# Kernel optimization log

Measured on AMD Instinct MI355X. Metric: run time of the kernel, lower is better.

## Reference

```python
import jax, jax.numpy as jnp
import numpy as np

N = 32768
DEG = 9        # 8 neighbors + self-loop
B = 8
K = 3          # Chebyshev degree
IN_CH = 8
OUT_CH = 2
HID = 64


def setup_inputs() -> dict:
    key = jax.random.key(0)
    ks = jax.random.split(key, 14)
    # structured 9-neighbor stencil (CSR-like sorted rows), honoring graph sparsity
    offs = np.arange(-4, 5)
    rows_np = np.repeat(np.arange(N), DEG).astype(np.int32)
    cols_np = ((rows_np.reshape(N, DEG) + offs[None, :]) % N).reshape(-1).astype(np.int32)
    vals = jax.random.normal(ks[0], (N * DEG,), jnp.float32) * 0.1
    x = jax.random.normal(ks[1], (B, N, IN_CH), jnp.float32)

    def w(k, fin, fout):
        return jax.random.normal(k, (K * fin, fout), jnp.float32) * 0.05

    def b(k, fout):
        return jax.random.normal(k, (fout,), jnp.float32) * 0.01

    return dict(
        x=x, rows=jnp.asarray(rows_np), cols=jnp.asarray(cols_np), vals=vals,
        W1=w(ks[2], IN_CH, HID), b1=b(ks[3], HID),
        W2=w(ks[4], HID, HID), b2=b(ks[5], HID),
        W3=w(ks[6], HID, HID), b3=b(ks[7], HID),
        W4=w(ks[8], HID, HID), b4=b(ks[9], HID),
        W5=w(ks[10], HID, OUT_CH), b5=b(ks[11], OUT_CH),
    )


def _spmm(rows, cols, vals, x):
    # sparse Laplacian @ x ; x: [B, N, C] -> [B, N, C]
    g = x[:, cols, :] * vals[None, :, None]          # [B, nnz, C]
    g = jnp.swapaxes(g, 0, 1)                        # [nnz, B, C]
    y = jax.ops.segment_sum(g, rows, num_segments=N) # [N, B, C]
    return jnp.swapaxes(y, 0, 1)


def _cheb_conv(rows, cols, vals, x, W, b):
    # Chebyshev recursion: T0 = x, T1 = L x, Tk = 2 L T_{k-1} - T_{k-2}
    x0 = x
    xs = [x0]
    if K > 1:
        x1 = _spmm(rows, cols, vals, x0)
        xs.append(x1)
        for _ in range(K - 2):
            x2 = 2.0 * _spmm(rows, cols, vals, x1) - x0
            xs.append(x2)
            x0, x1 = x1, x2
    xk = jnp.concatenate(xs, axis=-1)                # [B, N, K*Fin]
    return jnp.einsum('bnf,fo->bno', xk, W) + b


def reference(x, rows, cols, vals, W1, b1, W2, b2, W3, b3, W4, b4, W5, b5):
    h = jax.nn.elu(_cheb_conv(rows, cols, vals, x, W1, b1))
    h = jax.nn.elu(_cheb_conv(rows, cols, vals, h, W2, b2))
    h = jax.nn.elu(_cheb_conv(rows, cols, vals, h, W3, b3))
    h = jax.nn.elu(_cheb_conv(rows, cols, vals, h, W4, b4))
    out = _cheb_conv(rows, cols, vals, h, W5, b5)    # no ELU on last layer
    return out
```

## Files before the change

### kernel.cpp

```cpp
#include <hip/hip_runtime.h>
#include <math.h>

#define N_PIX 32768
#define DEG 9
#define BATCH 8
#define TILE 64

typedef unsigned short u16;
typedef __attribute__((ext_vector_type(8))) short bf16x8;
typedef __attribute__((ext_vector_type(16))) float f32x16;

__device__ __forceinline__ u16 bf16_rn(float x) {
    unsigned int u = __builtin_bit_cast(unsigned int, x);
    u += 0x7fffu + ((u >> 16) & 1u);
    return (u16)(u >> 16);
}
__device__ __forceinline__ float bf16_to_f(u16 u) {
    unsigned int v = ((unsigned int)u) << 16;
    return __builtin_bit_cast(float, v);
}


__global__ void prep_wt(const float* __restrict__ W2, const float* __restrict__ W3,
                        const float* __restrict__ W4, u16* __restrict__ out) {
    const float* W = (blockIdx.x == 0) ? W2 : (blockIdx.x == 1) ? W3 : W4;
    u16* o = out + (size_t)blockIdx.x * 24576;
    const int base = blockIdx.y * 768;
    for (int idx = base + threadIdx.x; idx < base + 768; idx += 256) {
        int j = idx & 7;
        int lane = (idx >> 3) & 63;
        int rest = idx >> 9;
        int s = rest & 3, tt = rest >> 2;
        int mt = tt & 1, mat = tt >> 1;
        int k = s * 16 + (lane >> 5) * 8 + j;
        int m = mt * 32 + (lane & 31);
        float x = (mat == 0) ? W[k * 64 + m] - W[(128 + k) * 64 + m]
                : (mat == 1) ? W[(64 + k) * 64 + m]
                             : W[(128 + k) * 64 + m];
        u16 hi = bf16_rn(x);
        o[idx] = hi;
        o[12288 + idx] = bf16_rn(x - bf16_to_f(hi));
    }
}

__global__ void prep_w1(const float* __restrict__ W1, u16* __restrict__ out) {
    u16* o = out + 73728;
    const int base = blockIdx.x * 1536;
    for (int e = base + threadIdx.x; e < base + 1536 && e < 24576; e += 256) {
        int j = e & 7;
        int lane = (e >> 3) & 63;
        int tt = e >> 12;
        int mt = tt & 1, mat = tt >> 1;
        int m = mt * 32 + (lane & 31);
        float x = 0.f;
        if ((lane >> 5) == 0) {
            x = (mat == 0) ? W1[j * 64 + m] - W1[(16 + j) * 64 + m]
              : (mat == 1) ? W1[(8 + j) * 64 + m]
                           : W1[(16 + j) * 64 + m];
        }
        u16 hi = bf16_rn(x);
        o[e] = hi;
        o[24576 + e] = bf16_rn(x - bf16_to_f(hi));
    }
}

template<bool FIRST>
__global__ __launch_bounds__(512, 6)
void cheb_conv(const float* __restrict__ Xf, const u16* __restrict__ Xh,
               const u16* __restrict__ Xl, const float* __restrict__ vals,
               const u16* __restrict__ wt, int wbase, const float* __restrict__ bias,
               u16* __restrict__ Yh, u16* __restrict__ Yl) {
    constexpr int LD = 68;
    __shared__ alignas(16) float P2s[80 * LD];
    __shared__ alignas(16) float P1s[72 * LD];
    __shared__ alignas(16) float Vs[72 * 12];

    const int tid = threadIdx.x;
    const int bx = ((blockIdx.x & 7) << 6) | (blockIdx.x >> 3);
    const int n0 = bx * TILE;
    const int b  = blockIdx.y;
    const size_t bplane = (size_t)b * ((size_t)N_PIX * 64);

    for (int i = tid; i < 648; i += 512) {
        int sr = i / 9, j = i - sr * 9;
        int g = (n0 - 4 + sr) & (N_PIX - 1);
        Vs[sr * 12 + j] = vals[(size_t)g * DEG + j];
    }

    const int w = tid >> 6, lane = tid & 63;
    const int half = lane >> 5, m31 = lane & 31;

    auto gemm_accs = [&](int mat, int rowoff, int rl, f32x16& acc0, f32x16& acc1) {
        const int g = (n0 + rowoff + rl) & (N_PIX - 1);
        constexpr int SC   = FIRST ? 1 : 4;
        constexpr int LOFF = FIRST ? 24576 : 12288;
        const u16* a0p = wt + wbase + lane * 8 + (FIRST ? (mat * 2) * 4096 : mat * 4096);
        const u16* a1p = a0p + (FIRST ? 4096 : 2048);
        const size_t bbase = bplane + (size_t)(g >> 5) * 2048 + (size_t)(g & 31) * 8;
        const float* xfp = FIRST ? (Xf + (size_t)b * N_PIX * 8 + (size_t)g * 8) : nullptr;
        #pragma unroll
        for (int s = 0; s < SC; ++s) {
            bf16x8 bh = {}, bl = {};
            if constexpr (FIRST) {
                if (half == 0) {
                    float xv[8];
                    *(float4*)&xv[0] = *(const float4*)&xfp[0];
                    *(float4*)&xv[4] = *(const float4*)&xfp[4];
                    #pragma unroll
                    for (int e = 0; e < 8; ++e) {
                        u16 hh = bf16_rn(xv[e]);
                        bh[e] = (short)hh;
                        bl[e] = (short)bf16_rn(xv[e] - bf16_to_f(hh));
                    }
                }
            } else {
                const size_t off = bbase + (size_t)(s * 2 + half) * 256;
                bh = *(const bf16x8*)&Xh[off];
                bl = *(const bf16x8*)&Xl[off];
            }
            bf16x8 a0h = *(const bf16x8*)(a0p + s * 512);
            bf16x8 a0l = *(const bf16x8*)(a0p + s * 512 + LOFF);
            bf16x8 a1h = *(const bf16x8*)(a1p + s * 512);
            bf16x8 a1l = *(const bf16x8*)(a1p + s * 512 + LOFF);
            acc0 = __builtin_amdgcn_mfma_f32_32x32x16_bf16(a0l, bh, acc0, 0, 0, 0);
            acc0 = __builtin_amdgcn_mfma_f32_32x32x16_bf16(a0h, bl, acc0, 0, 0, 0);
            acc0 = __builtin_amdgcn_mfma_f32_32x32x16_bf16(a0h, bh, acc0, 0, 0, 0);
            acc1 = __builtin_amdgcn_mfma_f32_32x32x16_bf16(a1l, bh, acc1, 0, 0, 0);
            acc1 = __builtin_amdgcn_mfma_f32_32x32x16_bf16(a1h, bl, acc1, 0, 0, 0);
            acc1 = __builtin_amdgcn_mfma_f32_32x32x16_bf16(a1h, bh, acc1, 0, 0, 0);
        }
    };
    auto scatter = [&](float* dst, int rl, const f32x16& a0, const f32x16& a1) {
        #pragma unroll
        for (int q = 0; q < 4; ++q) {
            float4 v0 = {a0[4 * q], a0[4 * q + 1], a0[4 * q + 2], a0[4 * q + 3]};
            float4 v1 = {a1[4 * q], a1[4 * q + 1], a1[4 * q + 2], a1[4 * q + 3]};
            *(float4*)&dst[rl * LD + q * 8 + half * 4]      = v0;
            *(float4*)&dst[rl * LD + 32 + q * 8 + half * 4] = v1;
        }
    };

    if (w < 6) {
        int mat, ntile, rowoff; float* dst;
        if (w < 3) { mat = 2; ntile = (w == 0) ? 0 : ((w == 1) ? 32 : 48); rowoff = -8; dst = P2s; }
        else       { mat = 1; ntile = (w == 3) ? 0 : ((w == 4) ? 32 : 40); rowoff = -4; dst = P1s; }
        f32x16 acc0 = {}, acc1 = {};
        gemm_accs(mat, rowoff, ntile + m31, acc0, acc1);
        scatter(dst, ntile + m31, acc0, acc1);
    }
    __syncthreads();

    f32x16 pacc0 = {}, pacc1 = {};
    int prl = 0;
    if (tid < 384) {
        const int st = tid >> 4, c0 = (tid & 15) << 2;
        const int r0 = st * 3;
        float4 win[11];
        #pragma unroll
        for (int l = 0; l < 11; ++l)
            win[l] = *(const float4*)&P2s[(r0 + l) * LD + c0];
        #pragma unroll
        for (int r = 0; r < 3; ++r) {
            const int sg = r0 + r;
            float4 vA = *(const float4*)&Vs[sg * 12];
            float4 vB = *(const float4*)&Vs[sg * 12 + 4];
            float v8 = Vs[sg * 12 + 8];
            const float vj[9] = {vA.x, vA.y, vA.z, vA.w, vB.x, vB.y, vB.z, vB.w, v8};
            float4 a = {0.f, 0.f, 0.f, 0.f};
            #pragma unroll
            for (int j = 0; j < 9; ++j) {
                float4 xv = win[r + j];
                a.x = fmaf(vj[j], xv.x, a.x); a.y = fmaf(vj[j], xv.y, a.y);
                a.z = fmaf(vj[j], xv.z, a.z); a.w = fmaf(vj[j], xv.w, a.w);
            }
            float4 p1 = *(const float4*)&P1s[sg * LD + c0];
            p1.x = fmaf(2.f, a.x, p1.x); p1.y = fmaf(2.f, a.y, p1.y);
            p1.z = fmaf(2.f, a.z, p1.z); p1.w = fmaf(2.f, a.w, p1.w);
            *(float4*)&P1s[sg * LD + c0] = p1;
        }
    } else {
        prl = ((w == 6) ? 0 : 32) + m31;
        gemm_accs(0, 0, prl, pacc0, pacc1);
    }
    __syncthreads();

    if (tid >= 384) scatter(P2s, prl, pacc0, pacc1);
    __syncthreads();

    {
        const int est = tid >> 4, ecx = tid & 15;
        const int ey0 = est * 2, ec0 = ecx << 2;
        float4 win[10];
        #pragma unroll
        for (int l = 0; l < 10; ++l)
            win[l] = *(const float4*)&P1s[(ey0 + l) * LD + ec0];
        const float4 bb = *(const float4*)&bias[ec0];
        #pragma unroll
        for (int r = 0; r < 2; ++r) {
            const int y = ey0 + r;
            float4 vA = *(const float4*)&Vs[(y + 4) * 12];
            float4 vB = *(const float4*)&Vs[(y + 4) * 12 + 4];
            float v8 = Vs[(y + 4) * 12 + 8];
            const float vj[9] = {vA.x, vA.y, vA.z, vA.w, vB.x, vB.y, vB.z, vB.w, v8};
            float4 a = bb;
            #pragma unroll
            for (int j = 0; j < 9; ++j) {
                float4 xv = win[r + j];
                a.x = fmaf(vj[j], xv.x, a.x); a.y = fmaf(vj[j], xv.y, a.y);
                a.z = fmaf(vj[j], xv.z, a.z); a.w = fmaf(vj[j], xv.w, a.w);
            }
            float4 p0 = *(const float4*)&P2s[y * LD + ec0];
            float yv[4] = {a.x + p0.x, a.y + p0.y, a.z + p0.z, a.w + p0.w};
            ushort4 h, l;
            u16 hh;
            #pragma unroll
            for (int e = 0; e < 4; ++e)
                yv[e] = yv[e] > 0.f ? yv[e] : __expf(yv[e]) - 1.f;
            hh = bf16_rn(yv[0]); h.x = hh; l.x = bf16_rn(yv[0] - bf16_to_f(hh));
            hh = bf16_rn(yv[1]); h.y = hh; l.y = bf16_rn(yv[1] - bf16_to_f(hh));
            hh = bf16_rn(yv[2]); h.z = hh; l.z = bf16_rn(yv[2] - bf16_to_f(hh));
            hh = bf16_rn(yv[3]); h.w = hh; l.w = bf16_rn(yv[3] - bf16_to_f(hh));
            const int gy = n0 + y;
            size_t dsto = bplane + (size_t)(gy >> 5) * 2048 + (size_t)(ecx >> 1) * 256
                        + (size_t)(gy & 31) * 8 + (size_t)(ecx & 1) * 4;
            *(ushort4*)&Yh[dsto] = h;
            *(ushort4*)&Yl[dsto] = l;
        }
    }
}

__global__ __launch_bounds__(256, 4)
void cheb_last3(const u16* __restrict__ Xh, const u16* __restrict__ Xl,
                const float* __restrict__ vals,
                const float* __restrict__ W5, const float* __restrict__ b5,
                float* __restrict__ Y) {
    __shared__ alignas(16) float Pb[80 * 8];
    __shared__ alignas(16) float Sb[72 * 2];
    __shared__ alignas(16) float Vs[72 * 12];

    const int tid = threadIdx.x;
    const int n0 = blockIdx.x * TILE;
    const int b  = blockIdx.y;
    const size_t bplane = (size_t)b * ((size_t)N_PIX * 64);

    for (int i = tid; i < 648; i += 256) {
        int sr = i / 9, j = i - sr * 9;
        int g = (n0 - 4 + sr) & (N_PIX - 1);
        Vs[sr * 12 + j] = vals[(size_t)g * DEG + j];
    }

    {
        const int w = tid >> 6, lane = tid & 63;
        const int half = lane >> 5, m31 = lane & 31;
        if (w < 3) {
            const int ntile = (w == 0) ? 0 : ((w == 1) ? 32 : 48);
            const int rl = ntile + m31;
            const int g = (n0 - 8 + rl) & (N_PIX - 1);
            const size_t bbase = bplane + (size_t)(g >> 5) * 2048 + (g & 31) * 8;
            const bool valid = m31 < 6;
            const int seg = m31 >> 1, o = m31 & 1;
            f32x16 acc = {};
            #pragma unroll
            for (int s = 0; s < 4; ++s) {
                const size_t off = bbase + (size_t)(s * 2 + half) * 256;
                bf16x8 bh = *(const bf16x8*)&Xh[off];
                bf16x8 bl = *(const bf16x8*)&Xl[off];
                bf16x8 ah, al;
                #pragma unroll
                for (int j = 0; j < 8; ++j) {
                    int k = s * 16 + half * 8 + j;
                    float x = valid ? W5[(seg * 64 + k) * 2 + o] : 0.f;
                    u16 hh = bf16_rn(x);
                    ah[j] = (short)hh;
                    al[j] = (short)bf16_rn(x - bf16_to_f(hh));
                }
                acc = __builtin_amdgcn_mfma_f32_32x32x16_bf16(al, bh, acc, 0, 0, 0);
                acc = __builtin_amdgcn_mfma_f32_32x32x16_bf16(ah, bl, acc, 0, 0, 0);
                acc = __builtin_amdgcn_mfma_f32_32x32x16_bf16(ah, bh, acc, 0, 0, 0);
            }
            if (half == 0) {
                float4 v = {acc[0], acc[1], acc[2], acc[3]};
                *(float4*)&Pb[rl * 8] = v;
            } else {
                Pb[rl * 8 + 4] = acc[0];
                Pb[rl * 8 + 5] = acc[1];
            }
        }
    }
    __syncthreads();

    if (tid < 144) {
        const int sg = tid >> 1, o = tid & 1;
        float q = 0.f;
        #pragma unroll
        for (int j = 0; j < DEG; ++j)
            q = fmaf(Vs[sg * 12 + j], Pb[(sg + j) * 8 + 4 + o], q);
        Sb[sg * 2 + o] = Pb[(sg + 4) * 8 + 2 + o] + 2.f * q;
    }
    __syncthreads();

    if (tid < 128) {
        const int y = tid >> 1, o = tid & 1;
        float q = 0.f;
        #pragma unroll
        for (int j = 0; j < DEG; ++j)
            q = fmaf(Vs[(y + 4) * 12 + j], Sb[(y + j) * 2 + o], q);
        float v = Pb[(y + 8) * 8 + o] - Pb[(y + 8) * 8 + 4 + o] + q + b5[o];
        Y[((size_t)b * N_PIX + n0 + y) * 2 + o] = v;
    }
}

extern "C" void kernel_launch(void* const* d_in, const int* in_sizes, int n_in,
                              void* d_out, int out_size, void* d_ws, size_t ws_size,
                              hipStream_t stream) {
    const float* x    = (const float*)d_in[0];
    const float* vals = (const float*)d_in[3];
    const float* W1 = (const float*)d_in[4];
    const float* b1 = (const float*)d_in[5];
    const float* W2 = (const float*)d_in[6];
    const float* b2 = (const float*)d_in[7];
    const float* W3 = (const float*)d_in[8];
    const float* b3 = (const float*)d_in[9];
    const float* W4 = (const float*)d_in[10];
    const float* b4 = (const float*)d_in[11];
    const float* W5 = (const float*)d_in[12];
    const float* b5 = (const float*)d_in[13];
    float* out = (float*)d_out;

    const size_t PL = (size_t)BATCH * N_PIX * 64;
    u16* Ah_g = (u16*)d_ws;
    u16* Al_g = Ah_g + PL;
    u16* Bh_g = Ah_g + 2 * PL;
    u16* Bl_g = Ah_g + 3 * PL;
    u16* wt = (u16*)d_out;

    dim3 grid(N_PIX / TILE, BATCH);
    prep_wt<<<dim3(3, 16), dim3(256), 0, stream>>>(W2, W3, W4, wt);
    prep_w1<<<dim3(16), dim3(256), 0, stream>>>(W1, wt);
    cheb_conv<true><<<grid, dim3(512), 0, stream>>>(x, nullptr, nullptr, vals, wt, 73728, b1, Ah_g, Al_g);
    cheb_conv<false><<<grid, dim3(512), 0, stream>>>(nullptr, Ah_g, Al_g, vals, wt, 0,     b2, Bh_g, Bl_g);
    cheb_conv<false><<<grid, dim3(512), 0, stream>>>(nullptr, Bh_g, Bl_g, vals, wt, 24576, b3, Ah_g, Al_g);
    cheb_conv<false><<<grid, dim3(512), 0, stream>>>(nullptr, Ah_g, Al_g, vals, wt, 49152, b4, Bh_g, Bl_g);
    cheb_last3<<<grid, dim3(256), 0, stream>>>(Bh_g, Bl_g, vals, W5, b5, out);
}
```

Before: 299.5 us.

## Merge prep kernels, pre-pad Laplacian values, and enlarge last-layer tiles

The two weight-prep kernels become one launch, which also writes the Laplacian values padded to 12 floats per row. That lets every cheb_conv block fill its shared values with aligned float4 loads instead of scalar loads with integer division. The final layer kernel now covers 128 pixels per block with 512 threads, so the 8-row halo is recomputed for fewer tiles. The padded values sit in the output buffer as scratch, and they and the packed weights must be written before the final kernel overwrites the output.

```diff
diff --git a/kernel.cpp b/kernel.cpp
--- a/kernel.cpp
+++ b/kernel.cpp
@@ -21,53 +21,64 @@
 }
 
 
-__global__ void prep_wt(const float* __restrict__ W2, const float* __restrict__ W3,
-                        const float* __restrict__ W4, u16* __restrict__ out) {
-    const float* W = (blockIdx.x == 0) ? W2 : (blockIdx.x == 1) ? W3 : W4;
-    u16* o = out + (size_t)blockIdx.x * 24576;
-    const int base = blockIdx.y * 768;
-    for (int idx = base + threadIdx.x; idx < base + 768; idx += 256) {
-        int j = idx & 7;
-        int lane = (idx >> 3) & 63;
-        int rest = idx >> 9;
-        int s = rest & 3, tt = rest >> 2;
-        int mt = tt & 1, mat = tt >> 1;
-        int k = s * 16 + (lane >> 5) * 8 + j;
-        int m = mt * 32 + (lane & 31);
-        float x = (mat == 0) ? W[k * 64 + m] - W[(128 + k) * 64 + m]
-                : (mat == 1) ? W[(64 + k) * 64 + m]
-                             : W[(128 + k) * 64 + m];
-        u16 hi = bf16_rn(x);
-        o[idx] = hi;
-        o[12288 + idx] = bf16_rn(x - bf16_to_f(hi));
-    }
-}
-
-__global__ void prep_w1(const float* __restrict__ W1, u16* __restrict__ out) {
-    u16* o = out + 73728;
-    const int base = blockIdx.x * 1536;
-    for (int e = base + threadIdx.x; e < base + 1536 && e < 24576; e += 256) {
-        int j = e & 7;
-        int lane = (e >> 3) & 63;
-        int tt = e >> 12;
-        int mt = tt & 1, mat = tt >> 1;
-        int m = mt * 32 + (lane & 31);
-        float x = 0.f;
-        if ((lane >> 5) == 0) {
-            x = (mat == 0) ? W1[j * 64 + m] - W1[(16 + j) * 64 + m]
-              : (mat == 1) ? W1[(8 + j) * 64 + m]
-                           : W1[(16 + j) * 64 + m];
-        }
-        u16 hi = bf16_rn(x);
-        o[e] = hi;
-        o[24576 + e] = bf16_rn(x - bf16_to_f(hi));
+__global__ void prep_all(const float* __restrict__ W1, const float* __restrict__ W2,
+                         const float* __restrict__ W3, const float* __restrict__ W4,
+                         const float* __restrict__ vals,
+                         u16* __restrict__ out, float* __restrict__ vpre) {
+    if (blockIdx.x < 3) {
+        const float* W = (blockIdx.x == 0) ? W2 : (blockIdx.x == 1) ? W3 : W4;
+        u16* o = out + (size_t)blockIdx.x * 24576;
+        const int base = blockIdx.y * 768;
+        for (int idx = base + threadIdx.x; idx < base + 768; idx += 256) {
+            int j = idx & 7;
+            int lane = (idx >> 3) & 63;
+            int rest = idx >> 9;
+            int s = rest & 3, tt = rest >> 2;
+            int mt = tt & 1, mat = tt >> 1;
+            int k = s * 16 + (lane >> 5) * 8 + j;
+            int m = mt * 32 + (lane & 31);
+            float x = (mat == 0) ? W[k * 64 + m] - W[(128 + k) * 64 + m]
+                    : (mat == 1) ? W[(64 + k) * 64 + m]
+                                 : W[(128 + k) * 64 + m];
+            u16 hi = bf16_rn(x);
+            o[idx] = hi;
+            o[12288 + idx] = bf16_rn(x - bf16_to_f(hi));
+        }
+    } else if (blockIdx.x == 3) {
+        u16* o = out + 73728;
+        const int base = blockIdx.y * 1536;
+        for (int e = base + threadIdx.x; e < base + 1536 && e < 24576; e += 256) {
+            int j = e & 7;
+            int lane = (e >> 3) & 63;
+            int tt = e >> 12;
+            int mt = tt & 1, mat = tt >> 1;
+            int m = mt * 32 + (lane & 31);
+            float x = 0.f;
+            if ((lane >> 5) == 0) {
+                x = (mat == 0) ? W1[j * 64 + m] - W1[(16 + j) * 64 + m]
+                  : (mat == 1) ? W1[(8 + j) * 64 + m]
+                               : W1[(16 + j) * 64 + m];
+            }
+            u16 hi = bf16_rn(x);
+            o[e] = hi;
+            o[24576 + e] = bf16_rn(x - bf16_to_f(hi));
+        }
+    } else if (blockIdx.x >= 5) {
+        const int vb = (blockIdx.x - 5) * 16 + blockIdx.y;
+        const int base = vb * 3072;
+        #pragma unroll
+        for (int k = 0; k < 12; ++k) {
+            int idx = base + k * 256 + threadIdx.x;
+            int g = idx / 12, j = idx - g * 12;
+            vpre[idx] = (j < 9) ? vals[(size_t)g * 9 + j] : 0.f;
+        }
     }
 }
 
 template<bool FIRST>
 __global__ __launch_bounds__(512, 6)
 void cheb_conv(const float* __restrict__ Xf, const u16* __restrict__ Xh,
-               const u16* __restrict__ Xl, const float* __restrict__ vals,
+               const u16* __restrict__ Xl, const float* __restrict__ Vpre,
                const u16* __restrict__ wt, int wbase, const float* __restrict__ bias,
                u16* __restrict__ Yh, u16* __restrict__ Yl) {
     constexpr int LD = 68;
@@ -81,10 +92,10 @@
     const int b  = blockIdx.y;
     const size_t bplane = (size_t)b * ((size_t)N_PIX * 64);
 
-    for (int i = tid; i < 648; i += 512) {
-        int sr = i / 9, j = i - sr * 9;
-        int g = (n0 - 4 + sr) & (N_PIX - 1);
-        Vs[sr * 12 + j] = vals[(size_t)g * DEG + j];
+    if (tid < 216) {
+        int r = tid / 3, q = tid - r * 3;
+        int g = (n0 - 4 + r) & (N_PIX - 1);
+        *(float4*)&Vs[r * 12 + q * 4] = *(const float4*)&Vpre[(size_t)g * 12 + q * 4];
     }
 
     const int w = tid >> 6, lane = tid & 63;
@@ -229,21 +240,21 @@
     }
 }
 
-__global__ __launch_bounds__(256, 4)
-void cheb_last3(const u16* __restrict__ Xh, const u16* __restrict__ Xl,
+__global__ __launch_bounds__(512, 4)
+void cheb_last4(const u16* __restrict__ Xh, const u16* __restrict__ Xl,
                 const float* __restrict__ vals,
                 const float* __restrict__ W5, const float* __restrict__ b5,
                 float* __restrict__ Y) {
-    __shared__ alignas(16) float Pb[80 * 8];
-    __shared__ alignas(16) float Sb[72 * 2];
-    __shared__ alignas(16) float Vs[72 * 12];
+    __shared__ alignas(16) float Pb[144 * 8];
+    __shared__ alignas(16) float Sb[136 * 2];
+    __shared__ alignas(16) float Vs[136 * 12];
 
     const int tid = threadIdx.x;
-    const int n0 = blockIdx.x * TILE;
+    const int n0 = blockIdx.x * 128;
     const int b  = blockIdx.y;
     const size_t bplane = (size_t)b * ((size_t)N_PIX * 64);
 
-    for (int i = tid; i < 648; i += 256) {
+    for (int i = tid; i < 1224; i += 512) {
         int sr = i / 9, j = i - sr * 9;
         int g = (n0 - 4 + sr) & (N_PIX - 1);
         Vs[sr * 12 + j] = vals[(size_t)g * DEG + j];
@@ -252,8 +263,8 @@
     {
         const int w = tid >> 6, lane = tid & 63;
         const int half = lane >> 5, m31 = lane & 31;
-        if (w < 3) {
-            const int ntile = (w == 0) ? 0 : ((w == 1) ? 32 : 48);
+        if (w < 5) {
+            const int ntile = (w == 4) ? 112 : w * 32;
             const int rl = ntile + m31;
             const int g = (n0 - 8 + rl) & (N_PIX - 1);
             const size_t bbase = bplane + (size_t)(g >> 5) * 2048 + (g & 31) * 8;
@@ -289,7 +300,7 @@
     }
     __syncthreads();
 
-    if (tid < 144) {
+    if (tid < 272) {
         const int sg = tid >> 1, o = tid & 1;
         float q = 0.f;
         #pragma unroll
@@ -299,7 +310,7 @@
     }
     __syncthreads();
 
-    if (tid < 128) {
+    if (tid < 256) {
         const int y = tid >> 1, o = tid & 1;
         float q = 0.f;
         #pragma unroll
@@ -333,13 +344,13 @@
     u16* Bh_g = Ah_g + 2 * PL;
     u16* Bl_g = Ah_g + 3 * PL;
     u16* wt = (u16*)d_out;
+    float* vpre = (float*)((char*)d_out + 262144);
 
     dim3 grid(N_PIX / TILE, BATCH);
-    prep_wt<<<dim3(3, 16), dim3(256), 0, stream>>>(W2, W3, W4, wt);
-    prep_w1<<<dim3(16), dim3(256), 0, stream>>>(W1, wt);
-    cheb_conv<true><<<grid, dim3(512), 0, stream>>>(x, nullptr, nullptr, vals, wt, 73728, b1, Ah_g, Al_g);
-    cheb_conv<false><<<grid, dim3(512), 0, stream>>>(nullptr, Ah_g, Al_g, vals, wt, 0,     b2, Bh_g, Bl_g);
-    cheb_conv<false><<<grid, dim3(512), 0, stream>>>(nullptr, Bh_g, Bl_g, vals, wt, 24576, b3, Ah_g, Al_g);
-    cheb_conv<false><<<grid, dim3(512), 0, stream>>>(nullptr, Ah_g, Al_g, vals, wt, 49152, b4, Bh_g, Bl_g);
-    cheb_last3<<<grid, dim3(256), 0, stream>>>(Bh_g, Bl_g, vals, W5, b5, out);
-}
+    prep_all<<<dim3(13, 16), dim3(256), 0, stream>>>(W1, W2, W3, W4, vals, wt, vpre);
+    cheb_conv<true><<<grid, dim3(512), 0, stream>>>(x, nullptr, nullptr, vpre, wt, 73728, b1, Ah_g, Al_g);
+    cheb_conv<false><<<grid, dim3(512), 0, stream>>>(nullptr, Ah_g, Al_g, vpre, wt, 0,     b2, Bh_g, Bl_g);
+    cheb_conv<false><<<grid, dim3(512), 0, stream>>>(nullptr, Bh_g, Bl_g, vpre, wt, 24576, b3, Ah_g, Al_g);
+    cheb_conv<false><<<grid, dim3(512), 0, stream>>>(nullptr, Ah_g, Al_g, vpre, wt, 49152, b4, Bh_g, Bl_g);
+    cheb_last4<<<dim3(N_PIX / 128, BATCH), dim3(512), 0, stream>>>(Bh_g, Bl_g, vals, W5, b5, out);
+}
```

Result: faster. 293.6 us (-2.0%).
